# Performance work log

Measured on AMD Instinct MI355X. Metric: run time of the kernel, lower is better.

Reference implementation:

```python
import jax, jax.numpy as jnp
import numpy as np

NQ, BS, NP_, D = 100, 8, 17, 256
NH, L, P = 8, 4, 4
DH = D // NH
DFF = 1024
SHAPES = [(92, 92), (46, 46), (23, 23), (12, 12)]
LEN_IN = sum(h * w for h, w in SHAPES)


def setup_inputs() -> dict:
    key = jax.random.key(0)
    ks = jax.random.split(key, 20)
    def nrm(k, shape, s=0.02):
        return jax.random.normal(k, shape, jnp.float32) * s
    return {
        "tgt_pose": jax.random.normal(ks[0], (NQ, BS, NP_, D), jnp.float32),
        "tgt_pose_query_pos": jax.random.normal(ks[1], (NQ, BS, NP_, D), jnp.float32),
        "tgt_pose_reference_points": jax.random.uniform(ks[2], (NQ, BS, NP_, L, 2), jnp.float32),
        "memory": jax.random.normal(ks[3], (BS, LEN_IN, D), jnp.float32),
        "w_in_w": nrm(ks[4], (3 * D, D)), "b_in_w": jnp.zeros((3 * D,), jnp.float32),
        "w_out_w": nrm(ks[5], (D, D)), "b_out_w": jnp.zeros((D,), jnp.float32),
        "w_in_a": nrm(ks[6], (3 * D, D)), "b_in_a": jnp.zeros((3 * D,), jnp.float32),
        "w_out_a": nrm(ks[7], (D, D)), "b_out_a": jnp.zeros((D,), jnp.float32),
        "w_off": nrm(ks[8], (NH * L * P * 2, D)), "b_off": nrm(ks[9], (NH * L * P * 2,), 0.1),
        "w_aw": nrm(ks[10], (NH * L * P, D)), "b_aw": jnp.zeros((NH * L * P,), jnp.float32),
        "w_val": nrm(ks[11], (D, D)), "b_val": jnp.zeros((D,), jnp.float32),
        "w_oc": nrm(ks[12], (D, D)), "b_oc": jnp.zeros((D,), jnp.float32),
        "g_w": jnp.ones((D,), jnp.float32), "be_w": jnp.zeros((D,), jnp.float32),
        "g_a": jnp.ones((D,), jnp.float32), "be_a": jnp.zeros((D,), jnp.float32),
        "g1": jnp.ones((D,), jnp.float32), "be1": jnp.zeros((D,), jnp.float32),
        "g2": jnp.ones((D,), jnp.float32), "be2": jnp.zeros((D,), jnp.float32),
        "w1": nrm(ks[13], (DFF, D)), "b1": jnp.zeros((DFF,), jnp.float32),
        "w2": nrm(ks[14], (D, DFF)), "b2": jnp.zeros((D,), jnp.float32),
        "memory_key_padding_mask": jnp.zeros((BS, LEN_IN), jnp.bool_),
        "memory_spatial_shapes": jnp.array(SHAPES, jnp.int32),
        "memory_level_start_index": jnp.array(np.cumsum([0] + [h * w for h, w in SHAPES[:-1]]), jnp.int32),
    }


def _ln(x, g, b, eps=1e-5):
    m = x.mean(-1, keepdims=True)
    v = ((x - m) ** 2).mean(-1, keepdims=True)
    return (x - m) * jax.lax.rsqrt(v + eps) * g + b


def _mha(q, k, v, w_in, b_in, w_out, b_out):
    # q,k,v: [B, S, D] batch-first; torch nn.MultiheadAttention math
    B, S, d = q.shape
    qp = (q @ w_in[:d].T + b_in[:d]).reshape(B, S, NH, DH)
    kp = (k @ w_in[d:2 * d].T + b_in[d:2 * d]).reshape(B, -1, NH, DH)
    vp = (v @ w_in[2 * d:].T + b_in[2 * d:]).reshape(B, -1, NH, DH)
    att = jax.nn.softmax(jnp.einsum('bqhd,bkhd->bhqk', qp, kp) / jnp.sqrt(jnp.float32(DH)), axis=-1)
    o = jnp.einsum('bhqk,bkhd->bqhd', att, vp).reshape(B, S, d)
    return o @ w_out.T + b_out


def _bilinear(v, loc, Hl, Wl):
    # v: [Hl*Wl, NH, DH]; loc: [Lq, NH, P, 2] normalized to [0,1]; grid_sample align_corners=False, zero pad
    x = loc[..., 0] * Wl - 0.5
    y = loc[..., 1] * Hl - 0.5
    x0 = jnp.floor(x); y0 = jnp.floor(y)
    wx = x - x0; wy = y - y0
    x0i = x0.astype(jnp.int32); y0i = y0.astype(jnp.int32)
    hid = jnp.arange(NH)[None, :, None]
    def tap(yi, xi, w):
        ok = (xi >= 0) & (xi < Wl) & (yi >= 0) & (yi < Hl)
        idx = jnp.clip(yi, 0, Hl - 1) * Wl + jnp.clip(xi, 0, Wl - 1)
        return jnp.where(ok[..., None], v[idx, hid], 0.0) * w[..., None]
    return (tap(y0i, x0i, (1 - wy) * (1 - wx)) + tap(y0i, x0i + 1, (1 - wy) * wx)
            + tap(y0i + 1, x0i, wy * (1 - wx)) + tap(y0i + 1, x0i + 1, wy * wx))


def _deform(query, ref, memory, mask, shapes, starts, w_off, b_off, w_aw, b_aw, w_val, b_val, w_oc, b_oc):
    # Multi-scale deformable attention (MSDeformAttn)
    bs, lq, d = query.shape
    value = memory @ w_val.T + b_val
    value = jnp.where(mask[..., None], 0.0, value).reshape(bs, -1, NH, DH)
    off = (query @ w_off.T + b_off).reshape(bs, lq, NH, L, P, 2)
    aw = jax.nn.softmax((query @ w_aw.T + b_aw).reshape(bs, lq, NH, L * P), axis=-1).reshape(bs, lq, NH, L, P)
    shp = np.asarray(shapes)
    st = np.asarray(starts)
    norm = jnp.asarray(shp[:, ::-1].copy(), jnp.float32)  # (W, H) per level
    loc = ref[:, :, None, :, None, :] + off / norm[None, None, None, :, None, :]
    out = jnp.zeros((bs, lq, NH, DH), query.dtype)
    for l in range(L):
        Hl, Wl = int(shp[l, 0]), int(shp[l, 1])
        v_l = value[:, int(st[l]):int(st[l]) + Hl * Wl]
        samp = jax.vmap(lambda vv, lo: _bilinear(vv, lo, Hl, Wl))(v_l, loc[:, :, :, l])
        out = out + jnp.einsum('bqhp,bqhpd->bqhd', aw[:, :, :, l], samp)
    return out.reshape(bs, lq, d) @ w_oc.T + b_oc


def _forward(tgt_pose, qpos, ref, memory, w_in_w, b_in_w, w_out_w, b_out_w, w_in_a, b_in_a, w_out_a, b_out_a, w_off, b_off, w_aw, b_aw, w_val, b_val, w_oc, b_oc, g_w, be_w, g_a, be_a, g1, be1, g2, be2, w1, b1, w2, b2, mask, shapes, starts):
    nq, bs, npt, d = tgt_pose.shape
    # within-group self-attn over keypoints (seq = np, batch = nq*bs)
    qk = (tgt_pose + qpos).reshape(nq * bs, npt, d)
    t2 = _mha(qk, qk, tgt_pose.reshape(nq * bs, npt, d), w_in_w, b_in_w, w_out_w, b_out_w).reshape(nq, bs, npt, d)
    x = _ln(tgt_pose + t2, g_w, be_w)
    # across-group self-attn over queries (seq = nq, batch = bs*np)
    y = x.reshape(nq, bs * npt, d).transpose(1, 0, 2)
    t2 = _mha(y, y, y, w_in_a, b_in_a, w_out_a, b_out_a).transpose(1, 0, 2).reshape(nq, bs, npt, d)
    x = _ln(x + t2, g_a, be_a)
    # multi-scale deformable cross-attn
    q = (x + qpos).transpose(1, 0, 2, 3).reshape(bs, nq * npt, d)
    r = ref.transpose(1, 0, 2, 3, 4).reshape(bs, nq * npt, L, 2)
    t2 = _deform(q, r, memory, mask, shapes, starts, w_off, b_off, w_aw, b_aw, w_val, b_val, w_oc, b_oc)
    t2 = t2.reshape(bs, nq, npt, d).transpose(1, 0, 2, 3)
    x = _ln(x + t2, g1, be1)
    # FFN
    ff = jax.nn.relu(x @ w1.T + b1) @ w2.T + b2
    return _ln(x + ff, g2, be2)


def reference(tgt_pose, tgt_pose_query_pos, tgt_pose_reference_points, memory, w_in_w, b_in_w, w_out_w, b_out_w, w_in_a, b_in_a, w_out_a, b_out_a, w_off, b_off, w_aw, b_aw, w_val, b_val, w_oc, b_oc, g_w, be_w, g_a, be_a, g1, be1, g2, be2, w1, b1, w2, b2, memory_key_padding_mask, memory_spatial_shapes, memory_level_start_index):
    return _forward(tgt_pose, tgt_pose_query_pos, tgt_pose_reference_points, memory, w_in_w, b_in_w, w_out_w, b_out_w, w_in_a, b_in_a, w_out_a, b_out_a, w_off, b_off, w_aw, b_aw, w_val, b_val, w_oc, b_oc, g_w, be_w, g_a, be_a, g1, be1, g2, be2, w1, b1, w2, b2, memory_key_padding_mask, memory_spatial_shapes, memory_level_start_index)
```

## Files before the change

kernel.cpp:

```cpp
#include <hip/hip_runtime.h>
#include <hip/hip_bf16.h>
#include <math.h>

#define NQd 100
#define BSd 8
#define NPTd 17
#define DIMd 256
#define NHd 8
#define DHd 32
#define DFFd 1024
#define NTOK (NQd*BSd*NPTd)
#define LENIN 11253
#define MTOK (BSd*LENIN)

typedef __attribute__((ext_vector_type(8))) short bf16x8;
typedef __attribute__((ext_vector_type(4))) short bf16x4s;
typedef __attribute__((ext_vector_type(4))) float f32x4;

__device__ inline short f2bs(float f) {
    __hip_bfloat16 h = __float2bfloat16(f);
    return *reinterpret_cast<short*>(&h);
}
__device__ inline float bs2f(short s) {
    return __uint_as_float(((unsigned)(unsigned short)s) << 16);
}
__device__ inline bf16x8 cvt8(const float* p) {
    float4 f0 = *(const float4*)p;
    float4 f1 = *(const float4*)(p + 4);
    return (bf16x8){f2bs(f0.x), f2bs(f0.y), f2bs(f0.z), f2bs(f0.w),
                    f2bs(f1.x), f2bs(f1.y), f2bs(f1.z), f2bs(f1.w)};
}

template<bool RELU, bool OUT_BF16, bool A_FP32>
__global__ __launch_bounds__(256)
void gemm_mfma(const void* __restrict__ Av, const __hip_bfloat16* __restrict__ W,
               const float* __restrict__ bias, void* __restrict__ Cv,
               int M, int N, int K, int ldc, int col0) {
    __shared__ __hip_bfloat16 LA[2][4][129][8];
    __shared__ __hip_bfloat16 LW[2][4][129][8];
    const int tid = threadIdx.x;
    const int lane = tid & 63, wave = tid >> 6;
    const int wr = wave >> 1, wc = wave & 1;
    const int m0 = blockIdx.y * 128, n0 = blockIdx.x * 128;
    const int l15 = lane & 15, lg = lane >> 4;
    const int srow = tid >> 2, koct = tid & 3;
    bf16x8 aReg[2], wReg[2];

    auto load_tile = [&](int k0) {
#pragma unroll
        for (int it = 0; it < 2; ++it) {
            const int row = srow + it * 64;
            const int gm = m0 + row;
            bf16x8 av = {0, 0, 0, 0, 0, 0, 0, 0};
            if (A_FP32) {
                if (gm < M) {
                    const float* ap = (const float*)Av + (size_t)gm * K + k0 + koct * 8;
                    float4 f0 = *(const float4*)ap;
                    float4 f1 = *(const float4*)(ap + 4);
                    av = (bf16x8){f2bs(f0.x), f2bs(f0.y), f2bs(f0.z), f2bs(f0.w),
                                  f2bs(f1.x), f2bs(f1.y), f2bs(f1.z), f2bs(f1.w)};
                }
            } else {
                if (gm < M)
                    av = *(const bf16x8*)((const __hip_bfloat16*)Av + (size_t)gm * K + k0 + koct * 8);
            }
            aReg[it] = av;
            wReg[it] = *(const bf16x8*)(W + (size_t)(n0 + row) * K + k0 + koct * 8);
        }
    };
    auto write_tile = [&](int buf) {
#pragma unroll
        for (int it = 0; it < 2; ++it) {
            const int row = srow + it * 64;
            *(bf16x8*)&LA[buf][koct][row][0] = aReg[it];
            *(bf16x8*)&LW[buf][koct][row][0] = wReg[it];
        }
    };

    f32x4 acc[4][4];
#pragma unroll
    for (int i = 0; i < 4; ++i)
#pragma unroll
        for (int j = 0; j < 4; ++j) acc[i][j] = (f32x4){0.f, 0.f, 0.f, 0.f};

    const int NT = K >> 5;
    load_tile(0);
    write_tile(0);
    __syncthreads();
    for (int t = 0; t < NT; ++t) {
        const int cur = t & 1;
        if (t + 1 < NT) load_tile((t + 1) * 32);
        bf16x8 af[4], bfr[4];
#pragma unroll
        for (int f = 0; f < 4; ++f) {
            af[f]  = *(const bf16x8*)&LA[cur][lg][wr * 64 + f * 16 + l15][0];
            bfr[f] = *(const bf16x8*)&LW[cur][lg][wc * 64 + f * 16 + l15][0];
        }
#pragma unroll
        for (int fm = 0; fm < 4; ++fm)
#pragma unroll
            for (int fn = 0; fn < 4; ++fn)
                acc[fm][fn] = __builtin_amdgcn_mfma_f32_16x16x32_bf16(af[fm], bfr[fn], acc[fm][fn], 0, 0, 0);
        if (t + 1 < NT) write_tile(cur ^ 1);
        __syncthreads();
    }

#pragma unroll
    for (int fm = 0; fm < 4; ++fm) {
        const int row = m0 + wr * 64 + fm * 16 + lg * 4;
#pragma unroll
        for (int fn = 0; fn < 4; ++fn) {
            const int coln = n0 + wc * 64 + fn * 16 + l15;
            const float bsv = bias[coln];
#pragma unroll
            for (int r = 0; r < 4; ++r) {
                const int gr = row + r;
                if (gr >= M) continue;
                float v = acc[fm][fn][r] + bsv;
                if (RELU) v = fmaxf(v, 0.f);
                if (OUT_BF16)
                    ((__hip_bfloat16*)Cv)[(size_t)gr * ldc + col0 + coln] = __float2bfloat16(v);
                else
                    ((float*)Cv)[(size_t)gr * ldc + col0 + coln] = v;
            }
        }
    }
}

template<bool A_FP32, bool OUT_BF16>
__global__ __launch_bounds__(256)
void gemm64(const void* __restrict__ Av, const __hip_bfloat16* __restrict__ W,
            const float* __restrict__ bias, void* __restrict__ Cv,
            int M, int K, int ldc, int col0) {
    __shared__ __hip_bfloat16 LA[2][4][65][8];
    __shared__ __hip_bfloat16 LW[2][4][65][8];
    const int tid = threadIdx.x;
    const int lane = tid & 63, wave = tid >> 6;
    const int wr = wave >> 1, wc = wave & 1;
    const int m0 = blockIdx.y * 64, n0 = blockIdx.x * 64;
    const int l15 = lane & 15, lg = lane >> 4;
    const int srow = tid >> 2, koct = tid & 3;
    const int gm = m0 + srow;
    const bool okA = gm < M;
    const __hip_bfloat16* pAb = (const __hip_bfloat16*)Av + (size_t)(okA ? gm : 0) * K + koct * 8;
    const float* pAf = (const float*)Av + (size_t)(okA ? gm : 0) * K + koct * 8;
    const __hip_bfloat16* pW = W + (size_t)(n0 + srow) * K + koct * 8;

    bf16x8 aR, wR;
    float4 f0R, f1R;
    auto load_tile = [&](int k0) {
        if (A_FP32) {
            f0R = okA ? *(const float4*)(pAf + k0)     : make_float4(0.f, 0.f, 0.f, 0.f);
            f1R = okA ? *(const float4*)(pAf + k0 + 4) : make_float4(0.f, 0.f, 0.f, 0.f);
        } else {
            aR = okA ? *(const bf16x8*)(pAb + k0) : (bf16x8){0, 0, 0, 0, 0, 0, 0, 0};
        }
        wR = *(const bf16x8*)(pW + k0);
    };
    auto write_tile = [&](int buf) {
        bf16x8 v;
        if (A_FP32)
            v = (bf16x8){f2bs(f0R.x), f2bs(f0R.y), f2bs(f0R.z), f2bs(f0R.w),
                         f2bs(f1R.x), f2bs(f1R.y), f2bs(f1R.z), f2bs(f1R.w)};
        else
            v = aR;
        *(bf16x8*)&LA[buf][koct][srow][0] = v;
        *(bf16x8*)&LW[buf][koct][srow][0] = wR;
    };

    f32x4 acc[2][2];
#pragma unroll
    for (int i = 0; i < 2; ++i)
#pragma unroll
        for (int j = 0; j < 2; ++j) acc[i][j] = (f32x4){0.f, 0.f, 0.f, 0.f};

    const int NT = K >> 5;
    load_tile(0);
    write_tile(0);
    __syncthreads();
    for (int t = 0; t < NT; ++t) {
        const int cur = t & 1;
        if (t + 1 < NT) load_tile((t + 1) * 32);
        bf16x8 af[2], bfr[2];
#pragma unroll
        for (int f = 0; f < 2; ++f) {
            af[f]  = *(const bf16x8*)&LA[cur][lg][wr * 32 + f * 16 + l15][0];
            bfr[f] = *(const bf16x8*)&LW[cur][lg][wc * 32 + f * 16 + l15][0];
        }
#pragma unroll
        for (int fm = 0; fm < 2; ++fm)
#pragma unroll
            for (int fn = 0; fn < 2; ++fn)
                acc[fm][fn] = __builtin_amdgcn_mfma_f32_16x16x32_bf16(af[fm], bfr[fn], acc[fm][fn], 0, 0, 0);
        if (t + 1 < NT) write_tile(cur ^ 1);
        __syncthreads();
    }

#pragma unroll
    for (int fm = 0; fm < 2; ++fm) {
        const int row = m0 + wr * 32 + fm * 16 + lg * 4;
#pragma unroll
        for (int fn = 0; fn < 2; ++fn) {
            const int coln = n0 + wc * 32 + fn * 16 + l15;
            const float bsv = bias[coln];
#pragma unroll
            for (int r = 0; r < 4; ++r) {
                const int gr = row + r;
                if (gr >= M) continue;
                float v = acc[fm][fn][r] + bsv;
                if (OUT_BF16)
                    ((__hip_bfloat16*)Cv)[(size_t)gr * ldc + col0 + coln] = __float2bfloat16(v);
                else
                    ((float*)Cv)[(size_t)gr * ldc + col0 + coln] = v;
            }
        }
    }
}

template<bool A_FP32, bool OUT_BF16>
__global__ __launch_bounds__(512)
void gemm64w(const void* __restrict__ Av, const __hip_bfloat16* __restrict__ W,
             const float* __restrict__ bias, void* __restrict__ Cv,
             int M, int K, int ldc, int col0) {
    __shared__ __hip_bfloat16 LA[2][4][65][8];
    const int tid = threadIdx.x;
    const int lane = tid & 63, wc = tid >> 6;
    const int m0 = blockIdx.x * 64;
    const int l15 = lane & 15, lg = lane >> 4;
    const int srow = (tid & 255) >> 2, koct = tid & 3;
    const bool stager = tid < 256;
    const int gm = m0 + srow;
    const bool okA = stager && (gm < M);
    const __hip_bfloat16* pAb = (const __hip_bfloat16*)Av + (size_t)(okA ? gm : 0) * K + koct * 8;
    const float* pAf = (const float*)Av + (size_t)(okA ? gm : 0) * K + koct * 8;
    const __hip_bfloat16* pW0 = W + (size_t)(wc * 32 + l15) * K + lg * 8;
    const __hip_bfloat16* pW1 = W + (size_t)(wc * 32 + 16 + l15) * K + lg * 8;

    bf16x8 aR;
    float4 f0R, f1R;
    auto load_tile = [&](int k0) {
        if (!stager) return;
        if (A_FP32) {
            f0R = okA ? *(const float4*)(pAf + k0)     : make_float4(0.f, 0.f, 0.f, 0.f);
            f1R = okA ? *(const float4*)(pAf + k0 + 4) : make_float4(0.f, 0.f, 0.f, 0.f);
        } else {
            aR = okA ? *(const bf16x8*)(pAb + k0) : (bf16x8){0, 0, 0, 0, 0, 0, 0, 0};
        }
    };
    auto write_tile = [&](int buf) {
        if (!stager) return;
        bf16x8 v;
        if (A_FP32)
            v = (bf16x8){f2bs(f0R.x), f2bs(f0R.y), f2bs(f0R.z), f2bs(f0R.w),
                         f2bs(f1R.x), f2bs(f1R.y), f2bs(f1R.z), f2bs(f1R.w)};
        else
            v = aR;
        *(bf16x8*)&LA[buf][koct][srow][0] = v;
    };

    f32x4 acc[4][2];
#pragma unroll
    for (int i = 0; i < 4; ++i) {
        acc[i][0] = (f32x4){0.f, 0.f, 0.f, 0.f};
        acc[i][1] = (f32x4){0.f, 0.f, 0.f, 0.f};
    }

    const int NT = K >> 5;
    load_tile(0);
    write_tile(0);
    __syncthreads();
    for (int t = 0; t < NT; ++t) {
        const int cur = t & 1;
        if (t + 1 < NT) load_tile((t + 1) * 32);
        bf16x8 b0 = *(const bf16x8*)(pW0 + t * 32);
        bf16x8 b1 = *(const bf16x8*)(pW1 + t * 32);
        bf16x8 af[4];
#pragma unroll
        for (int fm = 0; fm < 4; ++fm)
            af[fm] = *(const bf16x8*)&LA[cur][lg][fm * 16 + l15][0];
#pragma unroll
        for (int fm = 0; fm < 4; ++fm) {
            acc[fm][0] = __builtin_amdgcn_mfma_f32_16x16x32_bf16(af[fm], b0, acc[fm][0], 0, 0, 0);
            acc[fm][1] = __builtin_amdgcn_mfma_f32_16x16x32_bf16(af[fm], b1, acc[fm][1], 0, 0, 0);
        }
        if (t + 1 < NT) write_tile(cur ^ 1);
        __syncthreads();
    }

#pragma unroll
    for (int fm = 0; fm < 4; ++fm) {
        const int row = m0 + fm * 16 + lg * 4;
#pragma unroll
        for (int fn = 0; fn < 2; ++fn) {
            const int coln = wc * 32 + fn * 16 + l15;
            const float bsv = bias[coln];
#pragma unroll
            for (int r = 0; r < 4; ++r) {
                const int gr = row + r;
                if (gr >= M) continue;
                float v = acc[fm][fn][r] + bsv;
                if (OUT_BF16)
                    ((__hip_bfloat16*)Cv)[(size_t)gr * ldc + col0 + coln] = __float2bfloat16(v);
                else
                    ((float*)Cv)[(size_t)gr * ldc + col0 + coln] = v;
            }
        }
    }
}

__global__ void cvt_weights(const float* w0, const float* w1, const float* w2,
                            const float* w3, const float* w4, const float* w5,
                            const float* w6, const float* w7, const float* w8,
                            const float* w9, __hip_bfloat16* dst) {
    int idx = blockIdx.x * 256 + threadIdx.x;
    float v;
    if      (idx <  196608) v = w0[idx];
    else if (idx <  262144) v = w1[idx -  196608];
    else if (idx <  458752) v = w2[idx -  262144];
    else if (idx <  524288) v = w3[idx -  458752];
    else if (idx <  589824) v = w4[idx -  524288];
    else if (idx <  622592) v = w5[idx -  589824];
    else if (idx <  688128) v = w6[idx -  622592];
    else if (idx <  753664) v = w7[idx -  688128];
    else if (idx < 1015808) v = w8[idx -  753664];
    else                    v = w9[idx - 1015808];
    dst[idx] = __float2bfloat16(v);
}

__global__ void gather_rows_b(const float* __restrict__ src, const float* __restrict__ add,
                              __hip_bfloat16* __restrict__ dst, int mode) {
    int t = blockIdx.x, c = threadIdx.x;
    int r;
    if (mode == 0) r = t;
    else if (mode == 1) { int m = t / 100, q = t % 100; r = q * 136 + m; }
    else { int b = t / 1700, jj = t % 1700; int q = jj / 17, p = jj % 17; r = q * 136 + b * 17 + p; }
    float v = src[(size_t)r * 256 + c];
    if (add) v += add[(size_t)r * 256 + c];
    dst[(size_t)t * 256 + c] = __float2bfloat16(v);
}

__global__ void attn17(const float* __restrict__ qkv, __hip_bfloat16* __restrict__ out) {
    const int g = blockIdx.x, h = blockIdx.y;
    __shared__ float q[17][32], k[17][32], v[17][32], s[17][18];
    const int tid = threadIdx.x;
    for (int idx = tid; idx < 17 * 32; idx += 256) {
        int i = idx >> 5, d = idx & 31;
        size_t row = (size_t)(g * 17 + i) * 768 + h * 32 + d;
        q[i][d] = qkv[row];
        k[i][d] = qkv[row + 256];
        v[i][d] = qkv[row + 512];
    }
    __syncthreads();
    for (int idx = tid; idx < 17 * 17; idx += 256) {
        int i = idx / 17, j = idx % 17;
        float acc = 0.f;
#pragma unroll
        for (int d = 0; d < 32; ++d) acc += q[i][d] * k[j][d];
        s[i][j] = acc * 0.17677669529663688f;
    }
    __syncthreads();
    if (tid < 17) {
        float m = -1e30f;
        for (int j = 0; j < 17; ++j) m = fmaxf(m, s[tid][j]);
        float sum = 0.f;
        for (int j = 0; j < 17; ++j) { float e = __expf(s[tid][j] - m); s[tid][j] = e; sum += e; }
        float inv = 1.f / sum;
        for (int j = 0; j < 17; ++j) s[tid][j] *= inv;
    }
    __syncthreads();
    for (int idx = tid; idx < 17 * 32; idx += 256) {
        int i = idx >> 5, d = idx & 31;
        float acc = 0.f;
        for (int j = 0; j < 17; ++j) acc += s[i][j] * v[j][d];
        out[(size_t)(g * 17 + i) * 256 + h * 32 + d] = __float2bfloat16(acc);
    }
}

__global__ __launch_bounds__(128)
void attn100(const float* __restrict__ qkv, __hip_bfloat16* __restrict__ out) {
    const int g = blockIdx.x, h = blockIdx.y;
    __shared__ __hip_bfloat16 Vt[32][136];
    __shared__ __hip_bfloat16 Pl[2][16][136];
    const int tid = threadIdx.x;
    const int wave = tid >> 6, lane = tid & 63;
    const int l15 = lane & 15, lg = lane >> 4;

    for (int idx = tid; idx < 3200; idx += 128) {
        int j = idx >> 5, d = idx & 31;
        Vt[d][j] = __float2bfloat16(qkv[(size_t)(g * 100 + j) * 768 + 512 + h * 32 + d]);
    }
    for (int idx = tid; idx < 32 * 28; idx += 128) {
        int d = idx & 31, jz = 100 + (idx >> 5);
        Vt[d][jz] = __float2bfloat16(0.f);
    }
    __syncthreads();

    const int rt0 = wave ? 4 : 0, rt1 = wave ? 7 : 4;
    for (int rt = rt0; rt < rt1; ++rt) {
        const int rowbase = rt * 16;
        int qr = rowbase + l15; if (qr > 99) qr = 99;
        bf16x8 aq = cvt8(qkv + (size_t)(g * 100 + qr) * 768 + h * 32 + lg * 8);
        f32x4 s[7];
#pragma unroll
        for (int jt = 0; jt < 7; ++jt) {
            int jr = jt * 16 + l15; if (jr > 99) jr = 99;
            bf16x8 bk = cvt8(qkv + (size_t)(g * 100 + jr) * 768 + 256 + h * 32 + lg * 8);
            s[jt] = __builtin_amdgcn_mfma_f32_16x16x32_bf16(aq, bk, (f32x4){0.f, 0.f, 0.f, 0.f}, 0, 0, 0);
        }
        float mr[4] = {-1e30f, -1e30f, -1e30f, -1e30f};
#pragma unroll
        for (int jt = 0; jt < 7; ++jt) {
            const bool valid = (jt * 16 + l15) < 100;
#pragma unroll
            for (int r = 0; r < 4; ++r) {
                float v = valid ? s[jt][r] * 0.17677669529663688f : -1e30f;
                s[jt][r] = v;
                mr[r] = fmaxf(mr[r], v);
            }
        }
#pragma unroll
        for (int r = 0; r < 4; ++r) {
            mr[r] = fmaxf(mr[r], __shfl_xor(mr[r], 1));
            mr[r] = fmaxf(mr[r], __shfl_xor(mr[r], 2));
            mr[r] = fmaxf(mr[r], __shfl_xor(mr[r], 4));
            mr[r] = fmaxf(mr[r], __shfl_xor(mr[r], 8));
        }
        float lr[4] = {0.f, 0.f, 0.f, 0.f};
#pragma unroll
        for (int jt = 0; jt < 7; ++jt)
#pragma unroll
            for (int r = 0; r < 4; ++r) {
                float e = __expf(s[jt][r] - mr[r]);
                s[jt][r] = e;
                lr[r] += e;
            }
#pragma unroll
        for (int r = 0; r < 4; ++r) {
            lr[r] += __shfl_xor(lr[r], 1);
            lr[r] += __shfl_xor(lr[r], 2);
            lr[r] += __shfl_xor(lr[r], 4);
            lr[r] += __shfl_xor(lr[r], 8);
        }
#pragma unroll
        for (int jt = 0; jt < 7; ++jt)
#pragma unroll
            for (int r = 0; r < 4; ++r)
                Pl[wave][lg * 4 + r][jt * 16 + l15] = __float2bfloat16(s[jt][r]);
#pragma unroll
        for (int r = 0; r < 4; ++r)
            Pl[wave][lg * 4 + r][112 + l15] = __float2bfloat16(0.f);

        f32x4 o0 = (f32x4){0.f, 0.f, 0.f, 0.f};
        f32x4 o1 = (f32x4){0.f, 0.f, 0.f, 0.f};
#pragma unroll
        for (int c = 0; c < 4; ++c) {
            bf16x8 pa = *(const bf16x8*)&Pl[wave][l15][c * 32 + lg * 8];
            bf16x8 v0 = *(const bf16x8*)&Vt[l15][c * 32 + lg * 8];
            bf16x8 v1 = *(const bf16x8*)&Vt[16 + l15][c * 32 + lg * 8];
            o0 = __builtin_amdgcn_mfma_f32_16x16x32_bf16(pa, v0, o0, 0, 0, 0);
            o1 = __builtin_amdgcn_mfma_f32_16x16x32_bf16(pa, v1, o1, 0, 0, 0);
        }
#pragma unroll
        for (int r = 0; r < 4; ++r) {
            int row = rowbase + lg * 4 + r;
            if (row < 100) {
                float inv = 1.f / lr[r];
                __hip_bfloat16* op = out + (size_t)(g * 100 + row) * 256 + h * 32;
                op[l15]      = __float2bfloat16(o0[r] * inv);
                op[16 + l15] = __float2bfloat16(o1[r] * inv);
            }
        }
    }
}

#define TPB 4
__global__ __launch_bounds__(256)
void deform_sample(const __hip_bfloat16* __restrict__ value, const float* __restrict__ off,
                   const float* __restrict__ aw, const float* __restrict__ ref,
                   __hip_bfloat16* __restrict__ out) {
    const int t0 = blockIdx.x * TPB;
    const int tid = threadIdx.x;
    __shared__ float raw[TPB][128];
    __shared__ float wgt[TPB][128];
    __shared__ int   cidx[TPB][128][4];
    __shared__ float cw[TPB][128][4];

    for (int idx = tid; idx < TPB * 128; idx += 256) {
        int tk = idx >> 7, i = idx & 127;
        raw[tk][i] = aw[(size_t)(t0 + tk) * 128 + i];
    }
    __syncthreads();
    if (tid < TPB * 8) {
        int tk = tid >> 3, h = tid & 7;
        float m = -1e30f;
        for (int i = 0; i < 16; ++i) m = fmaxf(m, raw[tk][h * 16 + i]);
        float sum = 0.f;
        float e[16];
        for (int i = 0; i < 16; ++i) { e[i] = __expf(raw[tk][h * 16 + i] - m); sum += e[i]; }
        float inv = 1.f / sum;
        for (int i = 0; i < 16; ++i) wgt[tk][h * 16 + i] = e[i] * inv;
    }
    __syncthreads();

    const int Hs[4] = {92, 46, 23, 12};
    const int Sts[4] = {0, 8464, 10580, 11109};
    for (int s = tid; s < TPB * 128; s += 256) {
        int tk = s >> 7, sid = s & 127;
        int t = t0 + tk;
        int b = t / 1700, jj = t % 1700;
        int q = jj / 17, p = jj % 17;
        int l = (sid >> 2) & 3;
        int HW = Hs[l];
        float HWf = (float)HW;
        const float* refp = ref + (size_t)((q * 8 + b) * 17 + p) * 8;
        float rx = refp[l * 2], ry = refp[l * 2 + 1];
        float ox = off[(size_t)t * 256 + sid * 2];
        float oy = off[(size_t)t * 256 + sid * 2 + 1];
        float x = (rx + ox / HWf) * HWf - 0.5f;
        float y = (ry + oy / HWf) * HWf - 0.5f;
        float x0f = floorf(x), y0f = floorf(y);
        float wx = x - x0f, wy = y - y0f;
        int xi = (int)x0f, yi = (int)y0f;
        float wg = wgt[tk][sid];
#pragma unroll
        for (int c = 0; c < 4; ++c) {
            int cy = c >> 1, cx = c & 1;
            int yy = yi + cy, xx = xi + cx;
            bool ok = (xx >= 0) && (xx < HW) && (yy >= 0) && (yy < HW);
            int yc = min(max(yy, 0), HW - 1);
            int xc = min(max(xx, 0), HW - 1);
            cidx[tk][sid][c] = Sts[l] + yc * HW + xc;
            float w = (cy ? wy : 1.f - wy) * (cx ? wx : 1.f - wx);
            cw[tk][sid][c] = ok ? wg * w : 0.f;
        }
    }
    __syncthreads();

    const int tk = tid >> 6, lane = tid & 63;
    const int h = lane >> 3, d4 = (lane & 7) * 4;
    const int t = t0 + tk;
    const int b = t / 1700;
    const __hip_bfloat16* vb = value + (size_t)b * LENIN * 256 + h * 32 + d4;
    float4 acc = make_float4(0.f, 0.f, 0.f, 0.f);
    for (int s16 = 0; s16 < 16; ++s16) {
        int sid = h * 16 + s16;
#pragma unroll
        for (int c = 0; c < 4; ++c) {
            int idx = cidx[tk][sid][c];
            float w = cw[tk][sid][c];
            bf16x4s v = *(const bf16x4s*)(vb + (size_t)idx * 256);
            acc.x += w * bs2f(v.x); acc.y += w * bs2f(v.y);
            acc.z += w * bs2f(v.z); acc.w += w * bs2f(v.w);
        }
    }
    __hip_bfloat16* op = out + (size_t)t * 256 + h * 32 + d4;
    op[0] = __float2bfloat16(acc.x);
    op[1] = __float2bfloat16(acc.y);
    op[2] = __float2bfloat16(acc.z);
    op[3] = __float2bfloat16(acc.w);
}

__global__ __launch_bounds__(256)
void res_ln(const float* __restrict__ res, const float* __restrict__ proj,
            const float* __restrict__ g, const float* __restrict__ be,
            float* __restrict__ out, __hip_bfloat16* __restrict__ outb, int mode) {
    const int wave = threadIdx.x >> 6, lane = threadIdx.x & 63;
    const int r = blockIdx.x * 4 + wave;
    int t;
    if (mode == 0) t = r;
    else if (mode == 1) { int q = r / 136, m = r % 136; t = m * 100 + q; }
    else { int q = r / 136, rem = r % 136; int b = rem / 17, p = rem % 17; t = b * 1700 + q * 17 + p; }
    const int c4 = lane * 4;
    float4 a = *(const float4*)&res[(size_t)r * 256 + c4];
    float4 p = *(const float4*)&proj[(size_t)t * 256 + c4];
    float v[4] = {a.x + p.x, a.y + p.y, a.z + p.z, a.w + p.w};
    float s = v[0] + v[1] + v[2] + v[3];
#pragma unroll
    for (int off = 32; off > 0; off >>= 1) s += __shfl_xor(s, off);
    float mean = s * (1.f / 256.f);
    float d[4], ss = 0.f;
#pragma unroll
    for (int i = 0; i < 4; ++i) { d[i] = v[i] - mean; ss += d[i] * d[i]; }
#pragma unroll
    for (int off = 32; off > 0; off >>= 1) ss += __shfl_xor(ss, off);
    float rs = rsqrtf(ss * (1.f / 256.f) + 1e-5f);
    float4 gv = *(const float4*)&g[c4];
    float4 bv = *(const float4*)&be[c4];
    float o0 = d[0] * rs * gv.x + bv.x;
    float o1 = d[1] * rs * gv.y + bv.y;
    float o2 = d[2] * rs * gv.z + bv.z;
    float o3 = d[3] * rs * gv.w + bv.w;
    *(float4*)&out[(size_t)r * 256 + c4] = make_float4(o0, o1, o2, o3);
    if (outb) {
        bf16x4s ob = {f2bs(o0), f2bs(o1), f2bs(o2), f2bs(o3)};
        *(bf16x4s*)&outb[(size_t)r * 256 + c4] = ob;
    }
}

extern "C" void kernel_launch(void* const* d_in, const int* in_sizes, int n_in,
                              void* d_out, int out_size, void* d_ws, size_t ws_size,
                              hipStream_t stream) {
    const float* tgt    = (const float*)d_in[0];
    const float* qpos   = (const float*)d_in[1];
    const float* ref    = (const float*)d_in[2];
    const float* memory = (const float*)d_in[3];
    const float* w_in_w = (const float*)d_in[4];
    const float* b_in_w = (const float*)d_in[5];
    const float* w_out_w= (const float*)d_in[6];
    const float* b_out_w= (const float*)d_in[7];
    const float* w_in_a = (const float*)d_in[8];
    const float* b_in_a = (const float*)d_in[9];
    const float* w_out_a= (const float*)d_in[10];
    const float* b_out_a= (const float*)d_in[11];
    const float* w_off  = (const float*)d_in[12];
    const float* b_off  = (const float*)d_in[13];
    const float* w_aw   = (const float*)d_in[14];
    const float* b_aw   = (const float*)d_in[15];
    const float* w_val  = (const float*)d_in[16];
    const float* b_val  = (const float*)d_in[17];
    const float* w_oc   = (const float*)d_in[18];
    const float* b_oc   = (const float*)d_in[19];
    const float* g_w    = (const float*)d_in[20];
    const float* be_w   = (const float*)d_in[21];
    const float* g_a    = (const float*)d_in[22];
    const float* be_a   = (const float*)d_in[23];
    const float* g1     = (const float*)d_in[24];
    const float* be1    = (const float*)d_in[25];
    const float* g2     = (const float*)d_in[26];
    const float* be2    = (const float*)d_in[27];
    const float* w1     = (const float*)d_in[28];
    const float* b1     = (const float*)d_in[29];
    const float* w2     = (const float*)d_in[30];
    const float* b2     = (const float*)d_in[31];

    float* X  = (float*)d_out;
    float* ws = (float*)d_ws;
    float* R1 = ws;
    float* R2 = R1 + (size_t)MTOK * 256;
    float* R3 = R2 + (size_t)NTOK * 256;
    float* R6 = R3 + (size_t)NTOK * 128;
    float* QBF= R6 + (size_t)NTOK * 128;
    float* WBF= QBF+ (size_t)NTOK * 128;

    __hip_bfloat16* R3b = (__hip_bfloat16*)R3;
    __hip_bfloat16* Qb  = (__hip_bfloat16*)QBF;
    __hip_bfloat16* Wb  = (__hip_bfloat16*)WBF;
    __hip_bfloat16* Hb  = (__hip_bfloat16*)R1;
    __hip_bfloat16* Vb  = (__hip_bfloat16*)R1;

    __hip_bfloat16* w_in_w_b  = Wb;
    __hip_bfloat16* w_out_w_b = Wb +  196608;
    __hip_bfloat16* w_in_a_b  = Wb +  262144;
    __hip_bfloat16* w_out_a_b = Wb +  458752;
    __hip_bfloat16* w_off_b   = Wb +  524288;
    __hip_bfloat16* w_aw_b    = Wb +  589824;
    __hip_bfloat16* w_val_b   = Wb +  622592;
    __hip_bfloat16* w_oc_b    = Wb +  688128;
    __hip_bfloat16* w1_b      = Wb +  753664;
    __hip_bfloat16* w2_b      = Wb + 1015808;

    cvt_weights<<<4992, 256, 0, stream>>>(w_in_w, w_out_w, w_in_a, w_out_a, w_off,
                                          w_aw, w_val, w_oc, w1, w2, Wb);

    const int MY64 = (NTOK + 63) / 64;

    gather_rows_b<<<NTOK, 256, 0, stream>>>(tgt, qpos, Qb, 0);
    gemm_mfma<false, false, false><<<dim3(4, (NTOK + 127) / 128), 256, 0, stream>>>(
        Qb, w_in_w_b, b_in_w, R1, NTOK, 512, 256, 768, 0);
    gemm64<true, false><<<dim3(4, MY64), 256, 0, stream>>>(
        tgt, w_in_w_b + 512 * 256, b_in_w + 512, R1, NTOK, 256, 768, 512);
    attn17<<<dim3(800, 8), 256, 0, stream>>>(R1, R3b);
    gemm64<false, false><<<dim3(4, MY64), 256, 0, stream>>>(
        R3b, w_out_w_b, b_out_w, R2, NTOK, 256, 256, 0);
    res_ln<<<NTOK / 4, 256, 0, stream>>>(tgt, R2, g_w, be_w, X, nullptr, 0);

    gather_rows_b<<<NTOK, 256, 0, stream>>>(X, nullptr, Qb, 1);
    gemm_mfma<false, false, false><<<dim3(6, (NTOK + 127) / 128), 256, 0, stream>>>(
        Qb, w_in_a_b, b_in_a, R1, NTOK, 768, 256, 768, 0);
    attn100<<<dim3(136, 8), 128, 0, stream>>>(R1, R3b);
    gemm64<false, false><<<dim3(4, MY64), 256, 0, stream>>>(
        R3b, w_out_a_b, b_out_a, R2, NTOK, 256, 256, 0);
    res_ln<<<NTOK / 4, 256, 0, stream>>>(X, R2, g_a, be_a, X, nullptr, 1);

    gemm64w<true, true><<<(MTOK + 63) / 64, 512, 0, stream>>>(
        memory, w_val_b, b_val, Vb, MTOK, 256, 256, 0);
    gather_rows_b<<<NTOK, 256, 0, stream>>>(X, qpos, Qb, 2);
    gemm64<false, false><<<dim3(4, MY64), 256, 0, stream>>>(
        Qb, w_off_b, b_off, R2, NTOK, 256, 256, 0);
    gemm64<false, false><<<dim3(2, MY64), 256, 0, stream>>>(
        Qb, w_aw_b, b_aw, R6, NTOK, 256, 128, 0);
    deform_sample<<<NTOK / TPB, 256, 0, stream>>>(Vb, R2, R6, ref, R3b);
    gemm64<false, false><<<dim3(4, MY64), 256, 0, stream>>>(
        R3b, w_oc_b, b_oc, R2, NTOK, 256, 256, 0);
    res_ln<<<NTOK / 4, 256, 0, stream>>>(X, R2, g1, be1, X, Qb, 2);

    gemm_mfma<true, true, false><<<dim3(8, (NTOK + 127) / 128), 256, 0, stream>>>(
        Qb, w1_b, b1, Hb, NTOK, 1024, 256, 1024, 0);
    gemm64<false, false><<<dim3(4, MY64), 256, 0, stream>>>(
        (const __hip_bfloat16*)Hb, w2_b, b2, R2, NTOK, 1024, 256, 0);
    res_ln<<<NTOK / 4, 256, 0, stream>>>(X, R2, g2, be2, X, nullptr, 0);
}
```

Measured before the change: 333.8 us.

## Retile value-projection GEMM into 64x64 tiles with LDS-staged weights and XCD swizzle

Replaces the 512-thread value-projection GEMM, which used full-width 64x256 tiles with weights read straight from global memory, by a 256-thread 64x64-tile kernel. Both A and W tiles are now double-buffered in LDS, and each wave computes a 32x32 sub-tile. A block-index swizzle maps consecutive tiles onto the same XCD for L2 locality. This gives four times as many blocks and better occupancy, at the cost of re-reading the fp32 memory rows once per N tile.

```diff
diff --git a/kernel.cpp b/kernel.cpp
--- a/kernel.cpp
+++ b/kernel.cpp
@@ -217,53 +217,48 @@
     }
 }
 
-template<bool A_FP32, bool OUT_BF16>
-__global__ __launch_bounds__(512)
-void gemm64w(const void* __restrict__ Av, const __hip_bfloat16* __restrict__ W,
-             const float* __restrict__ bias, void* __restrict__ Cv,
-             int M, int K, int ldc, int col0) {
+__global__ __launch_bounds__(256)
+void gemm64x(const float* __restrict__ Av, const __hip_bfloat16* __restrict__ W,
+             const float* __restrict__ bias, __hip_bfloat16* __restrict__ Cv,
+             int M, int K, int ldc) {
+    const int nwg = gridDim.x;
+    const int orig = blockIdx.x;
+    const int xcd = orig & 7, loc = orig >> 3;
+    const int q = nwg >> 3, r = nwg & 7;
+    const int swz = (xcd < r ? xcd * (q + 1) : r * (q + 1) + (xcd - r) * q) + loc;
+    const int m0 = (swz >> 2) * 64, n0 = (swz & 3) * 64;
+
     __shared__ __hip_bfloat16 LA[2][4][65][8];
+    __shared__ __hip_bfloat16 LW[2][4][65][8];
     const int tid = threadIdx.x;
-    const int lane = tid & 63, wc = tid >> 6;
-    const int m0 = blockIdx.x * 64;
+    const int lane = tid & 63, wave = tid >> 6;
+    const int wr = wave >> 1, wc = wave & 1;
     const int l15 = lane & 15, lg = lane >> 4;
-    const int srow = (tid & 255) >> 2, koct = tid & 3;
-    const bool stager = tid < 256;
+    const int srow = tid >> 2, koct = tid & 3;
     const int gm = m0 + srow;
-    const bool okA = stager && (gm < M);
-    const __hip_bfloat16* pAb = (const __hip_bfloat16*)Av + (size_t)(okA ? gm : 0) * K + koct * 8;
-    const float* pAf = (const float*)Av + (size_t)(okA ? gm : 0) * K + koct * 8;
-    const __hip_bfloat16* pW0 = W + (size_t)(wc * 32 + l15) * K + lg * 8;
-    const __hip_bfloat16* pW1 = W + (size_t)(wc * 32 + 16 + l15) * K + lg * 8;
-
-    bf16x8 aR;
+    const bool okA = gm < M;
+    const float* pAf = Av + (size_t)(okA ? gm : 0) * K + koct * 8;
+    const __hip_bfloat16* pW = W + (size_t)(n0 + srow) * K + koct * 8;
+
+    bf16x8 wR;
     float4 f0R, f1R;
     auto load_tile = [&](int k0) {
-        if (!stager) return;
-        if (A_FP32) {
-            f0R = okA ? *(const float4*)(pAf + k0)     : make_float4(0.f, 0.f, 0.f, 0.f);
-            f1R = okA ? *(const float4*)(pAf + k0 + 4) : make_float4(0.f, 0.f, 0.f, 0.f);
-        } else {
-            aR = okA ? *(const bf16x8*)(pAb + k0) : (bf16x8){0, 0, 0, 0, 0, 0, 0, 0};
-        }
+        f0R = okA ? *(const float4*)(pAf + k0)     : make_float4(0.f, 0.f, 0.f, 0.f);
+        f1R = okA ? *(const float4*)(pAf + k0 + 4) : make_float4(0.f, 0.f, 0.f, 0.f);
+        wR = *(const bf16x8*)(pW + k0);
     };
     auto write_tile = [&](int buf) {
-        if (!stager) return;
-        bf16x8 v;
-        if (A_FP32)
-            v = (bf16x8){f2bs(f0R.x), f2bs(f0R.y), f2bs(f0R.z), f2bs(f0R.w),
-                         f2bs(f1R.x), f2bs(f1R.y), f2bs(f1R.z), f2bs(f1R.w)};
-        else
-            v = aR;
-        *(bf16x8*)&LA[buf][koct][srow][0] = v;
+        *(bf16x8*)&LA[buf][koct][srow][0] =
+            (bf16x8){f2bs(f0R.x), f2bs(f0R.y), f2bs(f0R.z), f2bs(f0R.w),
+                     f2bs(f1R.x), f2bs(f1R.y), f2bs(f1R.z), f2bs(f1R.w)};
+        *(bf16x8*)&LW[buf][koct][srow][0] = wR;
     };
 
-    f32x4 acc[4][2];
-#pragma unroll
-    for (int i = 0; i < 4; ++i) {
-        acc[i][0] = (f32x4){0.f, 0.f, 0.f, 0.f};
-        acc[i][1] = (f32x4){0.f, 0.f, 0.f, 0.f};
-    }
+    f32x4 acc[2][2];
+#pragma unroll
+    for (int i = 0; i < 2; ++i)
+#pragma unroll
+        for (int j = 0; j < 2; ++j) acc[i][j] = (f32x4){0.f, 0.f, 0.f, 0.f};
 
     const int NT = K >> 5;
     load_tile(0);
@@ -272,37 +267,33 @@
     for (int t = 0; t < NT; ++t) {
         const int cur = t & 1;
         if (t + 1 < NT) load_tile((t + 1) * 32);
-        bf16x8 b0 = *(const bf16x8*)(pW0 + t * 32);
-        bf16x8 b1 = *(const bf16x8*)(pW1 + t * 32);
-        bf16x8 af[4];
-#pragma unroll
-        for (int fm = 0; fm < 4; ++fm)
-            af[fm] = *(const bf16x8*)&LA[cur][lg][fm * 16 + l15][0];
-#pragma unroll
-        for (int fm = 0; fm < 4; ++fm) {
-            acc[fm][0] = __builtin_amdgcn_mfma_f32_16x16x32_bf16(af[fm], b0, acc[fm][0], 0, 0, 0);
-            acc[fm][1] = __builtin_amdgcn_mfma_f32_16x16x32_bf16(af[fm], b1, acc[fm][1], 0, 0, 0);
-        }
+        bf16x8 af[2], bfr[2];
+#pragma unroll
+        for (int f = 0; f < 2; ++f) {
+            af[f]  = *(const bf16x8*)&LA[cur][lg][wr * 32 + f * 16 + l15][0];
+            bfr[f] = *(const bf16x8*)&LW[cur][lg][wc * 32 + f * 16 + l15][0];
+        }
+#pragma unroll
+        for (int fm = 0; fm < 2; ++fm)
+#pragma unroll
+            for (int fn = 0; fn < 2; ++fn)
+                acc[fm][fn] = __builtin_amdgcn_mfma_f32_16x16x32_bf16(af[fm], bfr[fn], acc[fm][fn], 0, 0, 0);
         if (t + 1 < NT) write_tile(cur ^ 1);
         __syncthreads();
     }
 
 #pragma unroll
-    for (int fm = 0; fm < 4; ++fm) {
-        const int row = m0 + fm * 16 + lg * 4;
+    for (int fm = 0; fm < 2; ++fm) {
+        const int row = m0 + wr * 32 + fm * 16 + lg * 4;
 #pragma unroll
         for (int fn = 0; fn < 2; ++fn) {
-            const int coln = wc * 32 + fn * 16 + l15;
+            const int coln = n0 + wc * 32 + fn * 16 + l15;
             const float bsv = bias[coln];
 #pragma unroll
             for (int r = 0; r < 4; ++r) {
                 const int gr = row + r;
                 if (gr >= M) continue;
-                float v = acc[fm][fn][r] + bsv;
-                if (OUT_BF16)
-                    ((__hip_bfloat16*)Cv)[(size_t)gr * ldc + col0 + coln] = __float2bfloat16(v);
-                else
-                    ((float*)Cv)[(size_t)gr * ldc + col0 + coln] = v;
+                Cv[(size_t)gr * ldc + coln] = __float2bfloat16(acc[fm][fn][r] + bsv);
             }
         }
     }
@@ -682,8 +673,8 @@
         R3b, w_out_a_b, b_out_a, R2, NTOK, 256, 256, 0);
     res_ln<<<NTOK / 4, 256, 0, stream>>>(X, R2, g_a, be_a, X, nullptr, 1);
 
-    gemm64w<true, true><<<(MTOK + 63) / 64, 512, 0, stream>>>(
-        memory, w_val_b, b_val, Vb, MTOK, 256, 256, 0);
+    gemm64x<<<4 * ((MTOK + 63) / 64), 256, 0, stream>>>(
+        memory, w_val_b, b_val, Vb, MTOK, 256, 256);
     gather_rows_b<<<NTOK, 256, 0, stream>>>(X, qpos, Qb, 2);
     gemm64<false, false><<<dim3(4, MY64), 256, 0, stream>>>(
         Qb, w_off_b, b_off, R2, NTOK, 256, 256, 0);
```

Measured after the change: 329.7 us. Within noise of the previous version (-1.2%).
